# Kernel optimization log

Hardware: AMD Instinct MI355X
Metric: run time of the kernel (lower is better)

Reference implementation:

```python
import jax, jax.numpy as jnp
import numpy as np

N = 100000   # total nodes (types a: [0,50000), b: [50000,100000))
E = 500000   # edges per edge type
T = 4        # number of edge types
D_IN = 128
H = 4        # heads
F = 32       # out_feats per head
NEG_SLOPE = 0.2


def setup_inputs() -> dict:
    key = jax.random.key(0)
    ks = jax.random.split(key, 8)
    feat = jax.random.normal(ks[0], (N, D_IN), dtype=jnp.float32)
    src = jax.random.randint(ks[1], (T, E), 0, N)
    dst = jax.random.randint(ks[2], (T, E), 0, N)
    is_b = jnp.arange(N) >= (N // 2)  # node-type mask (type2mask)
    W = jax.random.normal(ks[3], (T, D_IN, H * F), dtype=jnp.float32) * (1.0 / np.sqrt(D_IN))
    attn_l = jax.random.normal(ks[4], (T, H, F), dtype=jnp.float32) * 0.1
    attn_r = jax.random.normal(ks[5], (T, H, F), dtype=jnp.float32) * 0.1
    W_merge = jax.random.normal(ks[6], (2 * H * F, F), dtype=jnp.float32) * (1.0 / np.sqrt(2 * H * F))
    b_merge = jax.random.normal(ks[7], (F,), dtype=jnp.float32) * 0.01
    return {"feat": feat, "src": src, "dst": dst, "is_b": is_b,
            "W": W, "attn_l": attn_l, "attn_r": attn_r,
            "W_merge": W_merge, "b_merge": b_merge}


def _gat_etype(feat, src_t, dst_t, W_t, al_t, ar_t):
    # Projected features: [N, H, F]
    ft = (feat @ W_t).reshape(N, H, F)
    el = jnp.einsum('nhf,hf->nh', ft, al_t)  # [N, H]
    er = jnp.einsum('nhf,hf->nh', ft, ar_t)  # [N, H]
    # u_add_v then LeakyReLU: [E, H]
    e = el[src_t] + er[dst_t]
    e = jnp.where(e > 0, e, NEG_SLOPE * e)
    # edge_softmax over incoming edges of each dst node (stable)
    m = jax.lax.stop_gradient(jax.ops.segment_max(e, dst_t, num_segments=N))
    ex = jnp.exp(e - m[dst_t])
    denom = jax.ops.segment_sum(ex, dst_t, num_segments=N)
    a = ex / denom[dst_t]  # [E, H]
    # u_mul_e + scatter-sum: [N, H, F]
    msg = ft[src_t] * a[:, :, None]
    out = jax.ops.segment_sum(msg, dst_t, num_segments=N)
    return out.reshape(N, H * F)


def reference(feat, src, dst, is_b, W, attn_l, attn_r, W_merge, b_merge):
    outs = [_gat_etype(feat, src[t], dst[t], W[t], attn_l[t], attn_r[t])
            for t in range(T)]
    # etypes dst order: a, a, b, b -> two per-etype feats per dst ntype
    feat_a = jnp.concatenate([outs[0], outs[1]], axis=1) @ W_merge + b_merge  # [N, F]
    feat_b = jnp.concatenate([outs[2], outs[3]], axis=1) @ W_merge + b_merge  # [N, F]
    # base_aggr_func: start with type-a result, overwrite type-b rows
    return jnp.where(is_b[:, None], feat_b, feat_a)
```

## Files before the change

kernel.cpp:

```cpp
#include <hip/hip_runtime.h>
#include <hip/hip_fp16.h>

typedef short short8 __attribute__((ext_vector_type(8)));
typedef _Float16 half8 __attribute__((ext_vector_type(8)));
typedef float f32x4 __attribute__((ext_vector_type(4)));

#define N_NODES 100000
#define N_A     50000
#define N_EDGES 500000
#define N_T     4
#define D_IN    128
#define HF      128
#define BCOLS   144
#define TN      (N_T * N_NODES)
#define TE      (N_T * N_EDGES)
#define NB1     ((TN + 1023) / 1024)
#define TILE_E  (BCOLS * D_IN)
#define LOG2E   1.44269504088896340736f

__device__ __forceinline__ unsigned short f2b(float f) {
  unsigned int u = __float_as_uint(f);
  u += 0x7FFFu + ((u >> 16) & 1u);
  return (unsigned short)(u >> 16);
}
__device__ __forceinline__ unsigned int pkh(float lo, float hi) {
  auto v = __builtin_amdgcn_cvt_pkrtz(lo, hi);
  unsigned int u; __builtin_memcpy(&u, &v, 4); return u;
}
__device__ __forceinline__ unsigned short f2h(float f) {
  auto v = __builtin_amdgcn_cvt_pkrtz(f, 0.f);
  unsigned int u; __builtin_memcpy(&u, &v, 4); return (unsigned short)(u & 0xFFFFu);
}
__device__ __forceinline__ __half2 w2h(unsigned int u) {
  __half2 h; __builtin_memcpy(&h, &u, 4); return h;
}
__device__ __forceinline__ unsigned int h2w(__half2 h) {
  unsigned int u; __builtin_memcpy(&u, &h, 4); return u;
}

__global__ __launch_bounds__(256) void k_prep(const float* __restrict__ W,
    const float* __restrict__ al, const float* __restrict__ ar,
    const float* __restrict__ Wm,
    unsigned short* __restrict__ Bt, unsigned short* __restrict__ WmT,
    int* __restrict__ cnt)
{
  if (blockIdx.x < 2) {
    int idx = blockIdx.x * 256 + threadIdx.x;
    int t = idx >> 7, k = idx & 127;
    const float* Wr = W + ((size_t)t * D_IN + k) * HF;
    unsigned short* o = Bt + (size_t)t * TILE_E;
    for (int j = 0; j < HF; ++j)
      o[(j * D_IN + k) ^ ((j & 7) << 3)] = f2b(Wr[j]);
    for (int h = 0; h < 4; ++h) {
      float sl = 0.f, sr = 0.f;
      const float* alh = al + (t * 4 + h) * 32;
      const float* arh = ar + (t * 4 + h) * 32;
      for (int f = 0; f < 32; ++f) { float w = Wr[h * 32 + f]; sl += w * alh[f]; sr += w * arh[f]; }
      int jl = 128 + h, jr = 132 + h;
      o[(jl * D_IN + k) ^ ((jl & 7) << 3)] = f2b(sl * LOG2E);
      o[(jr * D_IN + k) ^ ((jr & 7) << 3)] = f2b(sr * LOG2E);
    }
    for (int j = 136; j < 144; ++j)
      o[(j * D_IN + k) ^ ((j & 7) << 3)] = 0;
  } else {
    int idx = (blockIdx.x - 2) * 256 + threadIdx.x;
    int kidx = idx >> 5, j = idx & 31;
    int slot = kidx >> 7, p = kidx & 127;
    int col = (p & 7) * 16 + (p >> 3);
    WmT[j * 256 + kidx] = f2h(Wm[(slot * 128 + col) * 32 + j]);
  }
  for (int i = blockIdx.x * 256 + threadIdx.x; i < TN; i += 34 * 256)
    cnt[i] = 0;
}

__global__ __launch_bounds__(256, 4) void k_proj(const float* __restrict__ feat,
    const unsigned short* __restrict__ Btg,
    unsigned short* __restrict__ ftg,
    float* __restrict__ elg, float* __restrict__ erg)
{
  __shared__ __align__(16) unsigned short Bs[TILE_E];
  const int tid = threadIdx.x;
  const int wave = tid >> 6, lane = tid & 63;
  const int l15 = lane & 15, g = lane >> 4;
  const int wrow0 = blockIdx.x * 64 + wave * 16;

  short8 a[4];
  {
    int row = wrow0 + l15;
    const float* fr = feat + (size_t)(row < N_NODES ? row : N_NODES - 1) * D_IN;
#pragma unroll
    for (int kt = 0; kt < 4; ++kt) {
      float4 v0 = *(const float4*)(fr + kt * 32 + g * 8);
      float4 v1 = *(const float4*)(fr + kt * 32 + g * 8 + 4);
      short8 s;
      s[0] = (short)f2b(v0.x); s[1] = (short)f2b(v0.y);
      s[2] = (short)f2b(v0.z); s[3] = (short)f2b(v0.w);
      s[4] = (short)f2b(v1.x); s[5] = (short)f2b(v1.y);
      s[6] = (short)f2b(v1.z); s[7] = (short)f2b(v1.w);
      a[kt] = s;
    }
  }

  for (int t = 0; t < N_T; ++t) {
    if (t > 0) __syncthreads();
    {
      const uint4* src = (const uint4*)(Btg + (size_t)t * TILE_E);
      uint4* dstv = (uint4*)Bs;
#pragma unroll
      for (int i = 0; i < 9; ++i)
        dstv[i * 256 + tid] = src[i * 256 + tid];
    }
    __syncthreads();

    f32x4 acc[8];
#pragma unroll
    for (int ct = 0; ct < 8; ++ct) {
      f32x4 c = {0.f, 0.f, 0.f, 0.f};
#pragma unroll
      for (int kt = 0; kt < 4; ++kt) {
        int row = ct * 16 + l15;
        int boff = (row * 256 + kt * 64 + g * 16) ^ ((l15 & 7) << 4);
        short8 b = *(const short8*)((const char*)Bs + boff);
        c = __builtin_amdgcn_mfma_f32_16x16x32_bf16(a[kt], b, c, 0, 0, 0);
      }
      acc[ct] = c;
    }
    {
      f32x4 c8 = {0.f, 0.f, 0.f, 0.f};
#pragma unroll
      for (int kt = 0; kt < 4; ++kt) {
        int row = 128 + l15;
        int boff = (row * 256 + kt * 64 + g * 16) ^ ((l15 & 7) << 4);
        short8 b = *(const short8*)((const char*)Bs + boff);
        c8 = __builtin_amdgcn_mfma_f32_16x16x32_bf16(a[kt], b, c8, 0, 0, 0);
      }
      if (l15 < 8) {
#pragma unroll
        for (int r = 0; r < 4; ++r) {
          int row = wrow0 + g * 4 + r;
          if (row < N_NODES) {
            float v = c8[r];
            if (l15 < 4) elg[((size_t)t * N_NODES + row) * 4 + l15] = v;
            else         erg[((size_t)t * N_NODES + row) * 4 + (l15 - 4)] = v;
          }
        }
      }
    }
#pragma unroll
    for (int r = 0; r < 4; ++r) {
      int row = wrow0 + g * 4 + r;
      if (row < N_NODES) {
        uint4 o;
        o.x = pkh(acc[0][r], acc[1][r]);
        o.y = pkh(acc[2][r], acc[3][r]);
        o.z = pkh(acc[4][r], acc[5][r]);
        o.w = pkh(acc[6][r], acc[7][r]);
        *(uint4*)(ftg + ((size_t)t * N_NODES + row) * HF + l15 * 8) = o;
      }
    }
  }
}

__global__ __launch_bounds__(256) void k_hist(const int* __restrict__ dst,
    int* __restrict__ cnt, int* __restrict__ rank) {
  int idx = blockIdx.x * 256 + threadIdx.x;
  if (idx >= TE) return;
  int t = idx / N_EDGES;
  int d = dst[idx];
  bool keep = (t < 2) ? (d < N_A) : (d >= N_A);
  if (keep) rank[idx] = atomicAdd(&cnt[t * N_NODES + d], 1);
}

__global__ __launch_bounds__(256) void k_scan1(const int* __restrict__ cnt,
    int* __restrict__ ofs, int* __restrict__ bsum) {
  __shared__ int ts[256];
  int b = blockIdx.x, t = threadIdx.x;
  int base = b * 1024 + t * 4;
  int v0 = 0, v1 = 0, v2 = 0, v3 = 0;
  if (base + 0 < TN) v0 = cnt[base + 0];
  if (base + 1 < TN) v1 = cnt[base + 1];
  if (base + 2 < TN) v2 = cnt[base + 2];
  if (base + 3 < TN) v3 = cnt[base + 3];
  int s = v0 + v1 + v2 + v3;
  ts[t] = s;
  __syncthreads();
  for (int o = 1; o < 256; o <<= 1) {
    int x = (t >= o) ? ts[t - o] : 0;
    __syncthreads();
    ts[t] += x;
    __syncthreads();
  }
  int run = ts[t] - s;
  if (base + 0 < TN) ofs[base + 0] = run; run += v0;
  if (base + 1 < TN) ofs[base + 1] = run; run += v1;
  if (base + 2 < TN) ofs[base + 2] = run; run += v2;
  if (base + 3 < TN) ofs[base + 3] = run;
  if (t == 255) bsum[b] = ts[255];
}

__global__ __launch_bounds__(512) void k_scan2(int* __restrict__ bsum) {
  __shared__ int ts[512];
  int t = threadIdx.x;
  int v = (t < NB1) ? bsum[t] : 0;
  ts[t] = v;
  __syncthreads();
  for (int o = 1; o < 512; o <<= 1) {
    int x = (t >= o) ? ts[t - o] : 0;
    __syncthreads();
    ts[t] += x;
    __syncthreads();
  }
  if (t < NB1) bsum[t] = ts[t] - v;
}

__global__ __launch_bounds__(256) void k_scatter(const int* __restrict__ src, const int* __restrict__ dst,
    const int* __restrict__ ofs, const int* __restrict__ bsum, const int* __restrict__ rank,
    int* __restrict__ bkt) {
  int idx = blockIdx.x * 256 + threadIdx.x;
  if (idx >= TE) return;
  int t = idx / N_EDGES;
  int d = dst[idx];
  bool keep = (t < 2) ? (d < N_A) : (d >= N_A);
  if (!keep) return;
  int key = t * N_NODES + d;
  int p = ofs[key] + bsum[key >> 10] + rank[idx];
  bkt[p] = t * N_NODES + src[idx];
}

__global__ __launch_bounds__(256) void k_gathermerge(const int* __restrict__ bkt,
    const int* __restrict__ ofs, const int* __restrict__ cnt, const int* __restrict__ bsum,
    const float* __restrict__ elg, const float* __restrict__ erg,
    const uint4* __restrict__ ftu,
    const unsigned short* __restrict__ WmT, const float* __restrict__ bm,
    float* __restrict__ out)
{
  __shared__ __align__(16) unsigned short Al[16 * 264];
  int tid = threadIdx.x;
  int wave = tid >> 6, lane = tid & 63;
  int g8 = lane >> 3, l7 = lane & 7;
  int pidl = wave * 8 + g8;
  int pid = blockIdx.x * 32 + pidl;
  int n = pid >> 1, slot = pid & 1;
  int t = slot + ((n >= N_A) ? 2 : 0);
  int key = t * N_NODES + n;
  int base = ofs[key] + bsum[key >> 10];
  int c = cnt[key];
  float4 er4 = *(const float4*)(erg + (size_t)key * 4);
  __half2 A0 = __float2half2_rn(0.f), A1 = A0, A2 = A0, A3 = A0;
  __half2 B0 = A0, B1 = A0, B2 = A0, B3 = A0;
  float d0 = 0.f, d1 = 0.f, d2 = 0.f, d3 = 0.f;
  int qb = l7 * 2;
  for (int i = 0; i < c; i += 4) {
    bool v1 = i + 1 < c, v2 = i + 2 < c, v3 = i + 3 < c;
    int e0 = base + i;
    int e1 = base + (v1 ? i + 1 : i);
    int e2 = base + (v2 ? i + 2 : i);
    int e3 = base + (v3 ? i + 3 : i);
    int s0 = bkt[e0], s1 = bkt[e1], s2 = bkt[e2], s3 = bkt[e3];
    float4 eA = *(const float4*)(elg + (size_t)s0 * 4);
    float4 eB = *(const float4*)(elg + (size_t)s1 * 4);
    float4 eC = *(const float4*)(elg + (size_t)s2 * 4);
    float4 eD = *(const float4*)(elg + (size_t)s3 * 4);
    uint4 u0a = ftu[(size_t)s0 * 16 + qb], u0b = ftu[(size_t)s0 * 16 + qb + 1];
    uint4 u1a = ftu[(size_t)s1 * 16 + qb], u1b = ftu[(size_t)s1 * 16 + qb + 1];
    uint4 u2a = ftu[(size_t)s2 * 16 + qb], u2b = ftu[(size_t)s2 * 16 + qb + 1];
    uint4 u3a = ftu[(size_t)s3 * 16 + qb], u3b = ftu[(size_t)s3 * 16 + qb + 1];
    float s;
    float wa0, wa1, wa2, wa3, wb0, wb1, wb2, wb3;
    float wc0, wc1, wc2, wc3, wd0, wd1, wd2, wd3;
    s = eA.x + er4.x; wa0 = exp2f(fmaxf(s, 0.2f * s));
    s = eA.y + er4.y; wa1 = exp2f(fmaxf(s, 0.2f * s));
    s = eA.z + er4.z; wa2 = exp2f(fmaxf(s, 0.2f * s));
    s = eA.w + er4.w; wa3 = exp2f(fmaxf(s, 0.2f * s));
    s = eB.x + er4.x; wb0 = exp2f(fmaxf(s, 0.2f * s));
    s = eB.y + er4.y; wb1 = exp2f(fmaxf(s, 0.2f * s));
    s = eB.z + er4.z; wb2 = exp2f(fmaxf(s, 0.2f * s));
    s = eB.w + er4.w; wb3 = exp2f(fmaxf(s, 0.2f * s));
    s = eC.x + er4.x; wc0 = exp2f(fmaxf(s, 0.2f * s));
    s = eC.y + er4.y; wc1 = exp2f(fmaxf(s, 0.2f * s));
    s = eC.z + er4.z; wc2 = exp2f(fmaxf(s, 0.2f * s));
    s = eC.w + er4.w; wc3 = exp2f(fmaxf(s, 0.2f * s));
    s = eD.x + er4.x; wd0 = exp2f(fmaxf(s, 0.2f * s));
    s = eD.y + er4.y; wd1 = exp2f(fmaxf(s, 0.2f * s));
    s = eD.z + er4.z; wd2 = exp2f(fmaxf(s, 0.2f * s));
    s = eD.w + er4.w; wd3 = exp2f(fmaxf(s, 0.2f * s));
    if (!v1) { wb0 = wb1 = wb2 = wb3 = 0.f; }
    if (!v2) { wc0 = wc1 = wc2 = wc3 = 0.f; }
    if (!v3) { wd0 = wd1 = wd2 = wd3 = 0.f; }
    d0 += wa0 + wb0 + wc0 + wd0;
    d1 += wa1 + wb1 + wc1 + wd1;
    d2 += wa2 + wb2 + wc2 + wd2;
    d3 += wa3 + wb3 + wc3 + wd3;
    __half2 h0, h1, h2, h3;
    h0 = __float2half2_rn(wa0); h1 = __float2half2_rn(wa1);
    h2 = __float2half2_rn(wa2); h3 = __float2half2_rn(wa3);
    A0 = __hfma2(w2h(u0a.x), h0, A0); A1 = __hfma2(w2h(u0a.y), h1, A1);
    A2 = __hfma2(w2h(u0a.z), h2, A2); A3 = __hfma2(w2h(u0a.w), h3, A3);
    B0 = __hfma2(w2h(u0b.x), h0, B0); B1 = __hfma2(w2h(u0b.y), h1, B1);
    B2 = __hfma2(w2h(u0b.z), h2, B2); B3 = __hfma2(w2h(u0b.w), h3, B3);
    h0 = __float2half2_rn(wb0); h1 = __float2half2_rn(wb1);
    h2 = __float2half2_rn(wb2); h3 = __float2half2_rn(wb3);
    A0 = __hfma2(w2h(u1a.x), h0, A0); A1 = __hfma2(w2h(u1a.y), h1, A1);
    A2 = __hfma2(w2h(u1a.z), h2, A2); A3 = __hfma2(w2h(u1a.w), h3, A3);
    B0 = __hfma2(w2h(u1b.x), h0, B0); B1 = __hfma2(w2h(u1b.y), h1, B1);
    B2 = __hfma2(w2h(u1b.z), h2, B2); B3 = __hfma2(w2h(u1b.w), h3, B3);
    h0 = __float2half2_rn(wc0); h1 = __float2half2_rn(wc1);
    h2 = __float2half2_rn(wc2); h3 = __float2half2_rn(wc3);
    A0 = __hfma2(w2h(u2a.x), h0, A0); A1 = __hfma2(w2h(u2a.y), h1, A1);
    A2 = __hfma2(w2h(u2a.z), h2, A2); A3 = __hfma2(w2h(u2a.w), h3, A3);
    B0 = __hfma2(w2h(u2b.x), h0, B0); B1 = __hfma2(w2h(u2b.y), h1, B1);
    B2 = __hfma2(w2h(u2b.z), h2, B2); B3 = __hfma2(w2h(u2b.w), h3, B3);
    h0 = __float2half2_rn(wd0); h1 = __float2half2_rn(wd1);
    h2 = __float2half2_rn(wd2); h3 = __float2half2_rn(wd3);
    A0 = __hfma2(w2h(u3a.x), h0, A0); A1 = __hfma2(w2h(u3a.y), h1, A1);
    A2 = __hfma2(w2h(u3a.z), h2, A2); A3 = __hfma2(w2h(u3a.w), h3, A3);
    B0 = __hfma2(w2h(u3b.x), h0, B0); B1 = __hfma2(w2h(u3b.y), h1, B1);
    B2 = __hfma2(w2h(u3b.z), h2, B2); B3 = __hfma2(w2h(u3b.w), h3, B3);
  }
  __half2 i0 = __float2half2_rn((c > 0) ? 1.f / d0 : 0.f);
  __half2 i1 = __float2half2_rn((c > 0) ? 1.f / d1 : 0.f);
  __half2 i2 = __float2half2_rn((c > 0) ? 1.f / d2 : 0.f);
  __half2 i3 = __float2half2_rn((c > 0) ? 1.f / d3 : 0.f);
  uint4 oA, oB;
  oA.x = h2w(__hmul2(A0, i0)); oA.y = h2w(__hmul2(A1, i1));
  oA.z = h2w(__hmul2(A2, i2)); oA.w = h2w(__hmul2(A3, i3));
  oB.x = h2w(__hmul2(B0, i0)); oB.y = h2w(__hmul2(B1, i1));
  oB.z = h2w(__hmul2(B2, i2)); oB.w = h2w(__hmul2(B3, i3));
  int nl = pidl >> 1;
  *(uint4*)&Al[nl * 264 + slot * 128 + l7 * 16] = oA;
  *(uint4*)&Al[nl * 264 + slot * 128 + l7 * 16 + 8] = oB;
  __syncthreads();
  if (wave >= 2) return;

  int l15 = lane & 15, lk = (lane >> 4) * 8;
  f32x4 acc = {0.f, 0.f, 0.f, 0.f};
#pragma unroll
  for (int kt = 0; kt < 8; ++kt) {
    half8 a = *(const half8*)&Al[l15 * 264 + kt * 32 + lk];
    half8 b = *(const half8*)(const void*)(WmT + (size_t)(wave * 16 + l15) * 256 + kt * 32 + lk);
    acc = __builtin_amdgcn_mfma_f32_16x16x32_f16(a, b, acc, 0, 0, 0);
  }
  float bmv = bm[wave * 16 + l15];
#pragma unroll
  for (int r = 0; r < 4; ++r) {
    int row = blockIdx.x * 16 + (lane >> 4) * 4 + r;
    out[(size_t)row * 32 + wave * 16 + l15] = acc[r] + bmv;
  }
}

extern "C" void kernel_launch(void* const* d_in, const int* in_sizes, int n_in,
                              void* d_out, int out_size, void* d_ws, size_t ws_size,
                              hipStream_t stream)
{
  const float* feat = (const float*)d_in[0];
  const int*   src  = (const int*)d_in[1];
  const int*   dst  = (const int*)d_in[2];
  const float* W    = (const float*)d_in[4];
  const float* al   = (const float*)d_in[5];
  const float* ar   = (const float*)d_in[6];
  const float* Wm   = (const float*)d_in[7];
  const float* bm   = (const float*)d_in[8];
  float* out = (float*)d_out;
  (void)in_sizes; (void)n_in; (void)out_size; (void)ws_size;

  char* w = (char*)d_ws;
  size_t o = 0;
  auto take = [&](size_t bytes) -> void* {
    void* p = w + o;
    o += (bytes + 255) & ~(size_t)255;
    return p;
  };
  unsigned short* Btg = (unsigned short*)take((size_t)N_T * TILE_E * 2);
  unsigned short* WmT = (unsigned short*)take((size_t)32 * 256 * 2);
  unsigned short* ftg = (unsigned short*)take((size_t)TN * HF * 2);
  float* elg   = (float*)take((size_t)TN * 4 * 4);
  float* erg   = (float*)take((size_t)TN * 4 * 4);
  int*   cntb  = (int*)take((size_t)TN * 4);
  int*   ofs   = (int*)take((size_t)TN * 4);
  int*   bsum  = (int*)take(4096);
  int*   rank  = (int*)take((size_t)TE * 4);
  int*   bkt   = (int*)take((size_t)TE * 4);

  k_prep<<<34, 256, 0, stream>>>(W, al, ar, Wm, Btg, WmT, cntb);
  k_proj<<<1563, 256, 0, stream>>>(feat, Btg, ftg, elg, erg);
  k_hist<<<(TE + 255) / 256, 256, 0, stream>>>(dst, cntb, rank);
  k_scan1<<<NB1, 256, 0, stream>>>(cntb, ofs, bsum);
  k_scan2<<<1, 512, 0, stream>>>(bsum);
  k_scatter<<<(TE + 255) / 256, 256, 0, stream>>>(src, dst, ofs, bsum, rank, bkt);
  k_gathermerge<<<6250, 256, 0, stream>>>(bkt, ofs, cntb, bsum, elg, erg,
                                          (const uint4*)ftg, WmT, bm, out);
}
```

Baseline: 181.7 us.

## Aggregate raw features per head and fold W into merge matrix

Instead of projecting features per edge type (4x N x 128 fp16 tensors), the code keeps one fp16 copy of the raw input features and aggregates the attention-weighted raw features per head. It then applies a precomputed combined matrix (W_t times W_merge slice) in the final MFMA. The goal is to cut the projection GEMM and shrink the gathered feature table from four tensors to one, so L2 hit rates rise. In exchange each edge now does 4x as many half FMAs per lane (per-head accumulators), and the merge GEMM K dimension grows from 256 to 1024.

```diff
diff --git a/kernel.cpp b/kernel.cpp
--- a/kernel.cpp
+++ b/kernel.cpp
@@ -10,13 +10,11 @@
 #define N_EDGES 500000
 #define N_T     4
 #define D_IN    128
-#define HF      128
-#define BCOLS   144
 #define TN      (N_T * N_NODES)
 #define TE      (N_T * N_EDGES)
 #define NB1     ((TN + 1023) / 1024)
-#define TILE_E  (BCOLS * D_IN)
 #define LOG2E   1.44269504088896340736f
+#define ZSTR    1048
 
 __device__ __forceinline__ unsigned short f2b(float f) {
   unsigned int u = __float_as_uint(f);
@@ -41,53 +39,61 @@
 __global__ __launch_bounds__(256) void k_prep(const float* __restrict__ W,
     const float* __restrict__ al, const float* __restrict__ ar,
     const float* __restrict__ Wm,
-    unsigned short* __restrict__ Bt, unsigned short* __restrict__ WmT,
+    unsigned short* __restrict__ EBt, unsigned short* __restrict__ MT,
     int* __restrict__ cnt)
 {
-  if (blockIdx.x < 2) {
-    int idx = blockIdx.x * 256 + threadIdx.x;
-    int t = idx >> 7, k = idx & 127;
-    const float* Wr = W + ((size_t)t * D_IN + k) * HF;
-    unsigned short* o = Bt + (size_t)t * TILE_E;
-    for (int j = 0; j < HF; ++j)
-      o[(j * D_IN + k) ^ ((j & 7) << 3)] = f2b(Wr[j]);
-    for (int h = 0; h < 4; ++h) {
-      float sl = 0.f, sr = 0.f;
-      const float* alh = al + (t * 4 + h) * 32;
-      const float* arh = ar + (t * 4 + h) * 32;
-      for (int f = 0; f < 32; ++f) { float w = Wr[h * 32 + f]; sl += w * alh[f]; sr += w * arh[f]; }
-      int jl = 128 + h, jr = 132 + h;
-      o[(jl * D_IN + k) ^ ((jl & 7) << 3)] = f2b(sl * LOG2E);
-      o[(jr * D_IN + k) ^ ((jr & 7) << 3)] = f2b(sr * LOG2E);
-    }
-    for (int j = 136; j < 144; ++j)
-      o[(j * D_IN + k) ^ ((j & 7) << 3)] = 0;
+  if (blockIdx.x == 0) {
+    for (int o = threadIdx.x; o < 32 * 128; o += 256) {
+      int j = o >> 7, k = o & 127;
+      int jj = j & 15, tt = jj >> 2, h = jj & 3;
+      const float* av = (j < 16 ? al : ar) + (tt * 4 + h) * 32;
+      const float* Wr = W + ((size_t)tt * D_IN + k) * 128 + h * 32;
+      float s = 0.f;
+      for (int f = 0; f < 32; ++f) s += Wr[f] * av[f];
+      EBt[o ^ ((j & 7) << 3)] = f2b(s * LOG2E);
+    }
   } else {
-    int idx = (blockIdx.x - 2) * 256 + threadIdx.x;
-    int kidx = idx >> 5, j = idx & 31;
-    int slot = kidx >> 7, p = kidx & 127;
-    int col = (p & 7) * 16 + (p >> 3);
-    WmT[j * 256 + kidx] = f2h(Wm[(slot * 128 + col) * 32 + j]);
-  }
-  for (int i = blockIdx.x * 256 + threadIdx.x; i < TN; i += 34 * 256)
+    int base = (blockIdx.x - 1) * 2048 + threadIdx.x * 8;
+    for (int u = 0; u < 8; ++u) {
+      int o = base + u;
+      int type = o >> 15;
+      int j = (o >> 10) & 31;
+      int kidx = o & 1023;
+      int ts = kidx >> 9, h = (kidx >> 7) & 3, k = kidx & 127;
+      int t = type * 2 + ts;
+      const float* Wr = W + ((size_t)t * D_IN + k) * 128 + h * 32;
+      const float* Wmr = Wm + (size_t)(ts * 128 + h * 32) * 32 + j;
+      float s = 0.f;
+      for (int f = 0; f < 32; ++f) s += Wr[f] * Wmr[f * 32];
+      MT[(size_t)type * 32768 + j * 1024 + kidx] = f2h(s);
+    }
+  }
+  for (int i = blockIdx.x * 256 + threadIdx.x; i < TN; i += 33 * 256)
     cnt[i] = 0;
 }
 
 __global__ __launch_bounds__(256, 4) void k_proj(const float* __restrict__ feat,
-    const unsigned short* __restrict__ Btg,
-    unsigned short* __restrict__ ftg,
+    const unsigned short* __restrict__ EBt,
+    unsigned short* __restrict__ f16g,
     float* __restrict__ elg, float* __restrict__ erg)
 {
-  __shared__ __align__(16) unsigned short Bs[TILE_E];
+  __shared__ __align__(16) unsigned short EBs[32 * 128];
   const int tid = threadIdx.x;
   const int wave = tid >> 6, lane = tid & 63;
   const int l15 = lane & 15, g = lane >> 4;
   const int wrow0 = blockIdx.x * 64 + wave * 16;
 
+  {
+    const uint4* s = (const uint4*)EBt;
+    uint4* d = (uint4*)EBs;
+    for (int i = tid; i < 512; i += 256) d[i] = s[i];
+  }
+
   short8 a[4];
   {
     int row = wrow0 + l15;
-    const float* fr = feat + (size_t)(row < N_NODES ? row : N_NODES - 1) * D_IN;
+    bool ok = row < N_NODES;
+    const float* fr = feat + (size_t)(ok ? row : N_NODES - 1) * D_IN;
 #pragma unroll
     for (int kt = 0; kt < 4; ++kt) {
       float4 v0 = *(const float4*)(fr + kt * 32 + g * 8);
@@ -98,65 +104,33 @@
       s[4] = (short)f2b(v1.x); s[5] = (short)f2b(v1.y);
       s[6] = (short)f2b(v1.z); s[7] = (short)f2b(v1.w);
       a[kt] = s;
-    }
-  }
-
-  for (int t = 0; t < N_T; ++t) {
-    if (t > 0) __syncthreads();
-    {
-      const uint4* src = (const uint4*)(Btg + (size_t)t * TILE_E);
-      uint4* dstv = (uint4*)Bs;
-#pragma unroll
-      for (int i = 0; i < 9; ++i)
-        dstv[i * 256 + tid] = src[i * 256 + tid];
-    }
-    __syncthreads();
-
-    f32x4 acc[8];
-#pragma unroll
-    for (int ct = 0; ct < 8; ++ct) {
-      f32x4 c = {0.f, 0.f, 0.f, 0.f};
-#pragma unroll
-      for (int kt = 0; kt < 4; ++kt) {
-        int row = ct * 16 + l15;
-        int boff = (row * 256 + kt * 64 + g * 16) ^ ((l15 & 7) << 4);
-        short8 b = *(const short8*)((const char*)Bs + boff);
-        c = __builtin_amdgcn_mfma_f32_16x16x32_bf16(a[kt], b, c, 0, 0, 0);
+      if (ok) {
+        uint4 o;
+        o.x = pkh(v0.x, v0.y); o.y = pkh(v0.z, v0.w);
+        o.z = pkh(v1.x, v1.y); o.w = pkh(v1.z, v1.w);
+        ((uint4*)f16g)[(size_t)row * 16 + kt * 4 + g] = o;
       }
-      acc[ct] = c;
-    }
-    {
-      f32x4 c8 = {0.f, 0.f, 0.f, 0.f};
-#pragma unroll
-      for (int kt = 0; kt < 4; ++kt) {
-        int row = 128 + l15;
-        int boff = (row * 256 + kt * 64 + g * 16) ^ ((l15 & 7) << 4);
-        short8 b = *(const short8*)((const char*)Bs + boff);
-        c8 = __builtin_amdgcn_mfma_f32_16x16x32_bf16(a[kt], b, c8, 0, 0, 0);
-      }
-      if (l15 < 8) {
-#pragma unroll
-        for (int r = 0; r < 4; ++r) {
-          int row = wrow0 + g * 4 + r;
-          if (row < N_NODES) {
-            float v = c8[r];
-            if (l15 < 4) elg[((size_t)t * N_NODES + row) * 4 + l15] = v;
-            else         erg[((size_t)t * N_NODES + row) * 4 + (l15 - 4)] = v;
-          }
-        }
-      }
-    }
+    }
+  }
+  __syncthreads();
+
+#pragma unroll
+  for (int ct = 0; ct < 2; ++ct) {
+    f32x4 c = {0.f, 0.f, 0.f, 0.f};
+#pragma unroll
+    for (int kt = 0; kt < 4; ++kt) {
+      int brow = ct * 16 + l15;
+      int boff = (brow * 256 + kt * 64 + g * 16) ^ ((l15 & 7) << 4);
+      short8 b = *(const short8*)((const char*)EBs + boff);
+      c = __builtin_amdgcn_mfma_f32_16x16x32_bf16(a[kt], b, c, 0, 0, 0);
+    }
+    int tt = l15 >> 2, h = l15 & 3;
+    float* dstp = (ct == 0) ? elg : erg;
 #pragma unroll
     for (int r = 0; r < 4; ++r) {
-      int row = wrow0 + g * 4 + r;
-      if (row < N_NODES) {
-        uint4 o;
-        o.x = pkh(acc[0][r], acc[1][r]);
-        o.y = pkh(acc[2][r], acc[3][r]);
-        o.z = pkh(acc[4][r], acc[5][r]);
-        o.w = pkh(acc[6][r], acc[7][r]);
-        *(uint4*)(ftg + ((size_t)t * N_NODES + row) * HF + l15 * 8) = o;
-      }
+      int rw = wrow0 + g * 4 + r;
+      if (rw < N_NODES)
+        dstp[((size_t)tt * N_NODES + rw) * 4 + h] = c[r];
     }
   }
 }
@@ -224,127 +198,105 @@
   if (!keep) return;
   int key = t * N_NODES + d;
   int p = ofs[key] + bsum[key >> 10] + rank[idx];
-  bkt[p] = t * N_NODES + src[idx];
+  bkt[p] = src[idx];
 }
 
 __global__ __launch_bounds__(256) void k_gathermerge(const int* __restrict__ bkt,
     const int* __restrict__ ofs, const int* __restrict__ cnt, const int* __restrict__ bsum,
     const float* __restrict__ elg, const float* __restrict__ erg,
-    const uint4* __restrict__ ftu,
-    const unsigned short* __restrict__ WmT, const float* __restrict__ bm,
+    const uint4* __restrict__ f16g,
+    const unsigned short* __restrict__ MT, const float* __restrict__ bm,
     float* __restrict__ out)
 {
-  __shared__ __align__(16) unsigned short Al[16 * 264];
+  __shared__ __align__(16) unsigned short Zl[16 * ZSTR];
   int tid = threadIdx.x;
   int wave = tid >> 6, lane = tid & 63;
   int g8 = lane >> 3, l7 = lane & 7;
   int pidl = wave * 8 + g8;
-  int pid = blockIdx.x * 32 + pidl;
-  int n = pid >> 1, slot = pid & 1;
-  int t = slot + ((n >= N_A) ? 2 : 0);
+  int nl = pidl >> 1, tslot = pidl & 1;
+  int n = blockIdx.x * 16 + nl;
+  int type = (n >= N_A) ? 1 : 0;
+  int t = type * 2 + tslot;
   int key = t * N_NODES + n;
   int base = ofs[key] + bsum[key >> 10];
   int c = cnt[key];
+  int tb = t * N_NODES;
   float4 er4 = *(const float4*)(erg + (size_t)key * 4);
-  __half2 A0 = __float2half2_rn(0.f), A1 = A0, A2 = A0, A3 = A0;
-  __half2 B0 = A0, B1 = A0, B2 = A0, B3 = A0;
-  float d0 = 0.f, d1 = 0.f, d2 = 0.f, d3 = 0.f;
-  int qb = l7 * 2;
-  for (int i = 0; i < c; i += 4) {
-    bool v1 = i + 1 < c, v2 = i + 2 < c, v3 = i + 3 < c;
-    int e0 = base + i;
-    int e1 = base + (v1 ? i + 1 : i);
-    int e2 = base + (v2 ? i + 2 : i);
-    int e3 = base + (v3 ? i + 3 : i);
-    int s0 = bkt[e0], s1 = bkt[e1], s2 = bkt[e2], s3 = bkt[e3];
-    float4 eA = *(const float4*)(elg + (size_t)s0 * 4);
-    float4 eB = *(const float4*)(elg + (size_t)s1 * 4);
-    float4 eC = *(const float4*)(elg + (size_t)s2 * 4);
-    float4 eD = *(const float4*)(elg + (size_t)s3 * 4);
-    uint4 u0a = ftu[(size_t)s0 * 16 + qb], u0b = ftu[(size_t)s0 * 16 + qb + 1];
-    uint4 u1a = ftu[(size_t)s1 * 16 + qb], u1b = ftu[(size_t)s1 * 16 + qb + 1];
-    uint4 u2a = ftu[(size_t)s2 * 16 + qb], u2b = ftu[(size_t)s2 * 16 + qb + 1];
-    uint4 u3a = ftu[(size_t)s3 * 16 + qb], u3b = ftu[(size_t)s3 * 16 + qb + 1];
-    float s;
-    float wa0, wa1, wa2, wa3, wb0, wb1, wb2, wb3;
-    float wc0, wc1, wc2, wc3, wd0, wd1, wd2, wd3;
-    s = eA.x + er4.x; wa0 = exp2f(fmaxf(s, 0.2f * s));
-    s = eA.y + er4.y; wa1 = exp2f(fmaxf(s, 0.2f * s));
-    s = eA.z + er4.z; wa2 = exp2f(fmaxf(s, 0.2f * s));
-    s = eA.w + er4.w; wa3 = exp2f(fmaxf(s, 0.2f * s));
-    s = eB.x + er4.x; wb0 = exp2f(fmaxf(s, 0.2f * s));
-    s = eB.y + er4.y; wb1 = exp2f(fmaxf(s, 0.2f * s));
-    s = eB.z + er4.z; wb2 = exp2f(fmaxf(s, 0.2f * s));
-    s = eB.w + er4.w; wb3 = exp2f(fmaxf(s, 0.2f * s));
-    s = eC.x + er4.x; wc0 = exp2f(fmaxf(s, 0.2f * s));
-    s = eC.y + er4.y; wc1 = exp2f(fmaxf(s, 0.2f * s));
-    s = eC.z + er4.z; wc2 = exp2f(fmaxf(s, 0.2f * s));
-    s = eC.w + er4.w; wc3 = exp2f(fmaxf(s, 0.2f * s));
-    s = eD.x + er4.x; wd0 = exp2f(fmaxf(s, 0.2f * s));
-    s = eD.y + er4.y; wd1 = exp2f(fmaxf(s, 0.2f * s));
-    s = eD.z + er4.z; wd2 = exp2f(fmaxf(s, 0.2f * s));
-    s = eD.w + er4.w; wd3 = exp2f(fmaxf(s, 0.2f * s));
-    if (!v1) { wb0 = wb1 = wb2 = wb3 = 0.f; }
-    if (!v2) { wc0 = wc1 = wc2 = wc3 = 0.f; }
-    if (!v3) { wd0 = wd1 = wd2 = wd3 = 0.f; }
-    d0 += wa0 + wb0 + wc0 + wd0;
-    d1 += wa1 + wb1 + wc1 + wd1;
-    d2 += wa2 + wb2 + wc2 + wd2;
-    d3 += wa3 + wb3 + wc3 + wd3;
-    __half2 h0, h1, h2, h3;
-    h0 = __float2half2_rn(wa0); h1 = __float2half2_rn(wa1);
-    h2 = __float2half2_rn(wa2); h3 = __float2half2_rn(wa3);
-    A0 = __hfma2(w2h(u0a.x), h0, A0); A1 = __hfma2(w2h(u0a.y), h1, A1);
-    A2 = __hfma2(w2h(u0a.z), h2, A2); A3 = __hfma2(w2h(u0a.w), h3, A3);
-    B0 = __hfma2(w2h(u0b.x), h0, B0); B1 = __hfma2(w2h(u0b.y), h1, B1);
-    B2 = __hfma2(w2h(u0b.z), h2, B2); B3 = __hfma2(w2h(u0b.w), h3, B3);
-    h0 = __float2half2_rn(wb0); h1 = __float2half2_rn(wb1);
-    h2 = __float2half2_rn(wb2); h3 = __float2half2_rn(wb3);
-    A0 = __hfma2(w2h(u1a.x), h0, A0); A1 = __hfma2(w2h(u1a.y), h1, A1);
-    A2 = __hfma2(w2h(u1a.z), h2, A2); A3 = __hfma2(w2h(u1a.w), h3, A3);
-    B0 = __hfma2(w2h(u1b.x), h0, B0); B1 = __hfma2(w2h(u1b.y), h1, B1);
-    B2 = __hfma2(w2h(u1b.z), h2, B2); B3 = __hfma2(w2h(u1b.w), h3, B3);
-    h0 = __float2half2_rn(wc0); h1 = __float2half2_rn(wc1);
-    h2 = __float2half2_rn(wc2); h3 = __float2half2_rn(wc3);
-    A0 = __hfma2(w2h(u2a.x), h0, A0); A1 = __hfma2(w2h(u2a.y), h1, A1);
-    A2 = __hfma2(w2h(u2a.z), h2, A2); A3 = __hfma2(w2h(u2a.w), h3, A3);
-    B0 = __hfma2(w2h(u2b.x), h0, B0); B1 = __hfma2(w2h(u2b.y), h1, B1);
-    B2 = __hfma2(w2h(u2b.z), h2, B2); B3 = __hfma2(w2h(u2b.w), h3, B3);
-    h0 = __float2half2_rn(wd0); h1 = __float2half2_rn(wd1);
-    h2 = __float2half2_rn(wd2); h3 = __float2half2_rn(wd3);
-    A0 = __hfma2(w2h(u3a.x), h0, A0); A1 = __hfma2(w2h(u3a.y), h1, A1);
-    A2 = __hfma2(w2h(u3a.z), h2, A2); A3 = __hfma2(w2h(u3a.w), h3, A3);
-    B0 = __hfma2(w2h(u3b.x), h0, B0); B1 = __hfma2(w2h(u3b.y), h1, B1);
-    B2 = __hfma2(w2h(u3b.z), h2, B2); B3 = __hfma2(w2h(u3b.w), h3, B3);
-  }
-  __half2 i0 = __float2half2_rn((c > 0) ? 1.f / d0 : 0.f);
-  __half2 i1 = __float2half2_rn((c > 0) ? 1.f / d1 : 0.f);
-  __half2 i2 = __float2half2_rn((c > 0) ? 1.f / d2 : 0.f);
-  __half2 i3 = __float2half2_rn((c > 0) ? 1.f / d3 : 0.f);
-  uint4 oA, oB;
-  oA.x = h2w(__hmul2(A0, i0)); oA.y = h2w(__hmul2(A1, i1));
-  oA.z = h2w(__hmul2(A2, i2)); oA.w = h2w(__hmul2(A3, i3));
-  oB.x = h2w(__hmul2(B0, i0)); oB.y = h2w(__hmul2(B1, i1));
-  oB.z = h2w(__hmul2(B2, i2)); oB.w = h2w(__hmul2(B3, i3));
-  int nl = pidl >> 1;
-  *(uint4*)&Al[nl * 264 + slot * 128 + l7 * 16] = oA;
-  *(uint4*)&Al[nl * 264 + slot * 128 + l7 * 16 + 8] = oB;
+  __half2 z[4][8];
+#pragma unroll
+  for (int h = 0; h < 4; ++h)
+#pragma unroll
+    for (int q = 0; q < 8; ++q) z[h][q] = __float2half2_rn(0.f);
+  float dn[4] = {0.f, 0.f, 0.f, 0.f};
+
+#define EDGE_ACC(S)                                                         \
+  {                                                                         \
+    float4 el4 = *(const float4*)(elg + ((size_t)tb + (S)) * 4);            \
+    uint4 fa = f16g[(size_t)(S) * 16 + l7 * 2];                             \
+    uint4 fb = f16g[(size_t)(S) * 16 + l7 * 2 + 1];                         \
+    __half2 ch[8];                                                          \
+    ch[0] = w2h(fa.x); ch[1] = w2h(fa.y); ch[2] = w2h(fa.z); ch[3] = w2h(fa.w); \
+    ch[4] = w2h(fb.x); ch[5] = w2h(fb.y); ch[6] = w2h(fb.z); ch[7] = w2h(fb.w); \
+    float sv, wv[4];                                                        \
+    sv = el4.x + er4.x; wv[0] = exp2f(fmaxf(sv, 0.2f * sv));                \
+    sv = el4.y + er4.y; wv[1] = exp2f(fmaxf(sv, 0.2f * sv));                \
+    sv = el4.z + er4.z; wv[2] = exp2f(fmaxf(sv, 0.2f * sv));                \
+    sv = el4.w + er4.w; wv[3] = exp2f(fmaxf(sv, 0.2f * sv));                \
+    _Pragma("unroll")                                                       \
+    for (int h = 0; h < 4; ++h) {                                           \
+      dn[h] += wv[h];                                                       \
+      __half2 wh = __float2half2_rn(wv[h]);                                 \
+      _Pragma("unroll")                                                     \
+      for (int q = 0; q < 8; ++q) z[h][q] = __hfma2(ch[q], wh, z[h][q]);    \
+    }                                                                       \
+  }
+
+  int i = 0;
+  for (; i + 1 < c; i += 2) {
+    int s0 = bkt[base + i];
+    int s1 = bkt[base + i + 1];
+    EDGE_ACC(s0);
+    EDGE_ACC(s1);
+  }
+  if (i < c) {
+    int s0 = bkt[base + i];
+    EDGE_ACC(s0);
+  }
+#undef EDGE_ACC
+
+#pragma unroll
+  for (int h = 0; h < 4; ++h) {
+    __half2 iv = __float2half2_rn((c > 0) ? 1.f / dn[h] : 0.f);
+    uint4 oA, oB;
+    oA.x = h2w(__hmul2(z[h][0], iv)); oA.y = h2w(__hmul2(z[h][1], iv));
+    oA.z = h2w(__hmul2(z[h][2], iv)); oA.w = h2w(__hmul2(z[h][3], iv));
+    oB.x = h2w(__hmul2(z[h][4], iv)); oB.y = h2w(__hmul2(z[h][5], iv));
+    oB.z = h2w(__hmul2(z[h][6], iv)); oB.w = h2w(__hmul2(z[h][7], iv));
+    uint4* zp = (uint4*)Zl + nl * (ZSTR / 8) + tslot * 64 + h * 16 + l7 * 2;
+    zp[0] = oA;
+    zp[1] = oB;
+  }
   __syncthreads();
   if (wave >= 2) return;
 
-  int l15 = lane & 15, lk = (lane >> 4) * 8;
-  f32x4 acc = {0.f, 0.f, 0.f, 0.f};
-#pragma unroll
-  for (int kt = 0; kt < 8; ++kt) {
-    half8 a = *(const half8*)&Al[l15 * 264 + kt * 32 + lk];
-    half8 b = *(const half8*)(const void*)(WmT + (size_t)(wave * 16 + l15) * 256 + kt * 32 + lk);
-    acc = __builtin_amdgcn_mfma_f32_16x16x32_f16(a, b, acc, 0, 0, 0);
+  int l15 = lane & 15, gg = lane >> 4;
+  int bt = (blockIdx.x >= (N_A / 16)) ? 1 : 0;
+  const unsigned short* mt = MT + (size_t)bt * 32768 + (size_t)(wave * 16 + l15) * 1024;
+  f32x4 a0 = {0.f, 0.f, 0.f, 0.f}, a1 = {0.f, 0.f, 0.f, 0.f};
+#pragma unroll
+  for (int kt = 0; kt < 32; kt += 2) {
+    half8 av0 = *(const half8*)&Zl[l15 * ZSTR + kt * 32 + gg * 8];
+    half8 bv0 = *(const half8*)(mt + kt * 32 + gg * 8);
+    a0 = __builtin_amdgcn_mfma_f32_16x16x32_f16(av0, bv0, a0, 0, 0, 0);
+    half8 av1 = *(const half8*)&Zl[l15 * ZSTR + (kt + 1) * 32 + gg * 8];
+    half8 bv1 = *(const half8*)(mt + (kt + 1) * 32 + gg * 8);
+    a1 = __builtin_amdgcn_mfma_f32_16x16x32_f16(av1, bv1, a1, 0, 0, 0);
   }
   float bmv = bm[wave * 16 + l15];
 #pragma unroll
   for (int r = 0; r < 4; ++r) {
-    int row = blockIdx.x * 16 + (lane >> 4) * 4 + r;
-    out[(size_t)row * 32 + wave * 16 + l15] = acc[r] + bmv;
+    int row = blockIdx.x * 16 + gg * 4 + r;
+    out[(size_t)row * 32 + wave * 16 + l15] = a0[r] + a1[r] + bmv;
   }
 }
 
@@ -370,9 +322,9 @@
     o += (bytes + 255) & ~(size_t)255;
     return p;
   };
-  unsigned short* Btg = (unsigned short*)take((size_t)N_T * TILE_E * 2);
-  unsigned short* WmT = (unsigned short*)take((size_t)32 * 256 * 2);
-  unsigned short* ftg = (unsigned short*)take((size_t)TN * HF * 2);
+  unsigned short* EBt = (unsigned short*)take((size_t)32 * 128 * 2);
+  unsigned short* MT  = (unsigned short*)take((size_t)2 * 32 * 1024 * 2);
+  unsigned short* f16g= (unsigned short*)take((size_t)N_NODES * D_IN * 2);
   float* elg   = (float*)take((size_t)TN * 4 * 4);
   float* erg   = (float*)take((size_t)TN * 4 * 4);
   int*   cntb  = (int*)take((size_t)TN * 4);
@@ -381,12 +333,12 @@
   int*   rank  = (int*)take((size_t)TE * 4);
   int*   bkt   = (int*)take((size_t)TE * 4);
 
-  k_prep<<<34, 256, 0, stream>>>(W, al, ar, Wm, Btg, WmT, cntb);
-  k_proj<<<1563, 256, 0, stream>>>(feat, Btg, ftg, elg, erg);
+  k_prep<<<33, 256, 0, stream>>>(W, al, ar, Wm, EBt, MT, cntb);
+  k_proj<<<1563, 256, 0, stream>>>(feat, EBt, f16g, elg, erg);
   k_hist<<<(TE + 255) / 256, 256, 0, stream>>>(dst, cntb, rank);
   k_scan1<<<NB1, 256, 0, stream>>>(cntb, ofs, bsum);
   k_scan2<<<1, 512, 0, stream>>>(bsum);
   k_scatter<<<(TE + 255) / 256, 256, 0, stream>>>(src, dst, ofs, bsum, rank, bkt);
   k_gathermerge<<<6250, 256, 0, stream>>>(bkt, ofs, cntb, bsum, elg, erg,
-                                          (const uint4*)ftg, WmT, bm, out);
-}
+                                          (const uint4*)f16g, MT, bm, out);
+}
```

Result: slower. 200.7 us (+10.5%).
